# Optimization experiments

Measured on AMD Instinct MI355X. Metric: run time of the kernel, lower is better.

## Reference

```python
import jax, jax.numpy as jnp
import numpy as np

U = 512   # units
D = 512   # decoder input feature dim
V = 46    # output vocab


def _lstm_cell(x_t, h, c, W, R, b):
    # Keras LSTMCell: gate order i, f, g(cell), o; sigmoid recurrent act, tanh act.
    z = x_t @ W + h @ R + b                      # [B, 4U]
    i, f, g, o = jnp.split(z, 4, axis=-1)
    i = jax.nn.sigmoid(i)
    f = jax.nn.sigmoid(f)
    g = jnp.tanh(g)
    o = jax.nn.sigmoid(o)
    c_new = f * c + i * g
    h_new = o * jnp.tanh(c_new)
    return h_new, c_new


def _lstm_seq(seq, W, R, b):
    # seq: [T, B, D]; zero initial state (Keras default). Returns (all h [T,B,U], last h [B,U]).
    B = seq.shape[1]
    u = R.shape[0]
    h0 = jnp.zeros((B, u), seq.dtype)
    c0 = jnp.zeros((B, u), seq.dtype)
    def step(carry, x_t):
        h, c = carry
        h, c = _lstm_cell(x_t, h, c, W, R, b)
        return (h, c), h
    (hT, _), hs = jax.lax.scan(step, (h0, c0), seq)
    return hs, hT


def setup_inputs() -> dict:
    key = jax.random.key(0)
    ks = jax.random.split(key, 10)
    def p(k, shape, scale=0.05):
        return jax.random.normal(k, shape, dtype=jnp.float32) * scale
    x = jax.random.normal(ks[0], (32, 512, U), dtype=jnp.float32)   # encoder outputs [B, S, U]
    y = jax.random.normal(ks[1], (32, 128, D), dtype=jnp.float32)   # decoder inputs  [B, T, D]
    return {
        "x": x, "y": y,
        "W_a": p(ks[2], (D, 4 * U)), "R_a": p(ks[3], (U, 4 * U)), "b_a": jnp.zeros((4 * U,), jnp.float32),
        "W1": p(ks[4], (U, 4 * U)), "R1": p(ks[5], (U, 4 * U)), "b1": jnp.zeros((4 * U,), jnp.float32),
        "W2": p(ks[6], (U, 4 * U)), "R2": p(ks[7], (U, 4 * U)), "b2": jnp.zeros((4 * U,), jnp.float32),
        "Wd": p(ks[8], (U, V)), "bd": jnp.zeros((V,), jnp.float32),
    }


def reference(x, y, W_a, R_a, b_a, W1, R1, b1, W2, R2, b2, Wd, bd):
    B = y.shape[0]
    yT = jnp.swapaxes(y, 0, 1)                          # [T, B, D]
    h0 = jnp.zeros((B, U), x.dtype)
    c0 = jnp.zeros((B, U), x.dtype)

    # AttentionLSTM: per-step LSTMCell + dot-product attention (Keras Attention,
    # unscaled, keys==values==x) + residual add of the context into both states.
    def step(carry, y_t):
        h, c = carry
        h, c = _lstm_cell(y_t, h, c, W_a, R_a, b_a)     # s = h  [B, U]
        scores = jnp.einsum('bu,bsu->bs', h, x)         # [B, S]
        ctx = jnp.einsum('bs,bsu->bu', jax.nn.softmax(scores, axis=-1), x)  # [B, U]
        return (h + ctx, c + ctx), ctx

    _, ctxs = jax.lax.scan(step, (h0, c0), yT)          # [T, B, U]

    # Stacked LSTMs: first returns full sequence, second returns last hidden state.
    hs1, _ = _lstm_seq(ctxs, W1, R1, b1)                # [T, B, U]
    _, hT = _lstm_seq(hs1, W2, R2, b2)                  # [B, U]

    logits = hT @ Wd + bd                               # [B, V]
    return jax.nn.softmax(logits, axis=-1)
```

## Files before the change

### kernel.cpp

```cpp
#include <hip/hip_runtime.h>
#include <math.h>


#define U_   512
#define S_   512
#define T_   128
#define B_   32
#define G4   2048
#define V_   46
#define NWG  256
#define FSTR 32

#define AT_LD(p)     __hip_atomic_load((p), __ATOMIC_RELAXED, __HIP_MEMORY_SCOPE_AGENT)
#define AT_ST(p, v)  __hip_atomic_store((p), (v), __ATOMIC_RELAXED, __HIP_MEMORY_SCOPE_AGENT)

__device__ __forceinline__ void group_bar(unsigned* gflags, unsigned seq) {
  __syncthreads();
  const int tid = threadIdx.x;
  if (tid < 32) {
    if (tid == 0)
      AT_ST(&gflags[(blockIdx.x & 31) * FSTR], seq);
    while (!__all(AT_LD(&gflags[tid * FSTR]) >= seq))
      __builtin_amdgcn_s_sleep(1);
  }
  __syncthreads();
}

__global__ __launch_bounds__(256) void gemm_k512(
    const float* __restrict__ A, const float* __restrict__ W,
    const float* __restrict__ b, float* __restrict__ Z) {
  const int tid = threadIdx.x;
  const int j = blockIdx.x * 1024 + tid * 4;
  const int i0 = blockIdx.y * 8;
  float4 bj = *(const float4*)(b + j);
  float4 acc[8];
#pragma unroll
  for (int r = 0; r < 8; ++r) acc[r] = bj;
  const float* Arow = A + (size_t)i0 * U_;
  for (int k = 0; k < U_; ++k) {
    float4 w = *(const float4*)(W + (size_t)k * G4 + j);
#pragma unroll
    for (int r = 0; r < 8; ++r) {
      float a = Arow[(size_t)r * U_ + k];
      acc[r].x = fmaf(a, w.x, acc[r].x);
      acc[r].y = fmaf(a, w.y, acc[r].y);
      acc[r].z = fmaf(a, w.z, acc[r].z);
      acc[r].w = fmaf(a, w.w, acc[r].w);
    }
  }
#pragma unroll
  for (int r = 0; r < 8; ++r)
    *(float4*)(Z + (size_t)(i0 + r) * G4 + j) = acc[r];
}

__global__ __launch_bounds__(256) void transpose_R(
    const float* __restrict__ R, float* __restrict__ RT) {
  __shared__ float tile[64][65];
  const int c0 = blockIdx.x * 64, k0 = blockIdx.y * 64;
  const int tc = threadIdx.x & 63, tr = threadIdx.x >> 6;
  for (int r = tr; r < 64; r += 4)
    tile[r][tc] = R[(size_t)(k0 + r) * G4 + c0 + tc];
  __syncthreads();
  for (int r = tr; r < 64; r += 4)
    RT[(size_t)(c0 + r) * 512 + k0 + tc] = tile[tc][r];
}

__global__ __launch_bounds__(512) void attn_coop(
    const float* __restrict__ x, const float* __restrict__ ZY,
    const float* __restrict__ RT, float* __restrict__ ctxs,
    float* hbuf, float* hnbuf, float* smax, float* ssumg,
    float* ctxpart, unsigned* flags) {
  extern __shared__ float dyn[];
  float* x_s  = dyn;
  float* h_st = dyn + 512 * 65;
  __shared__ float zp[4][64][2];
  __shared__ float hn_s[512];
  __shared__ float p_s[64];
  __shared__ float ctx_s[64];

  const int tid = threadIdx.x;
  const int bid = blockIdx.x;
  const int g    = bid >> 5;
  const int wgid = bid & 31;
  const int u0   = wgid * 16;
  const int kh  = tid & 1;
  const int b_l = (tid >> 1) & 3;
  const int col = tid >> 3;
  const int zcol = (col >> 4) * 512 + u0 + (col & 15);
  const int b_att = 4 * g + (wgid >> 3);
  const int sc = wgid & 7;
  unsigned* gflags = flags + g * 32 * FSTR;

  for (int idx = tid; idx < 64 * 512; idx += 512) {
    int sl = idx >> 9, u = idx & 511;
    x_s[u * 65 + sl] = x[((size_t)b_att * S_ + sc * 64 + sl) * U_ + u];
  }
  float c = 0.f, hn_reg = 0.f;
  unsigned seq = 0;
  __syncthreads();

  for (int t = 0; t < T_; ++t) {
    {
      const float4* hb4 =
          (const float4*)(hbuf + (size_t)t * 16384 + 4 * g * 512);
      float4 v = hb4[tid];
      *(float4*)(h_st + (tid >> 7) * 516 + (tid & 127) * 4) = v;
    }
    __syncthreads();
    {
      const float4* H4 = (const float4*)(h_st + b_l * 516 + kh * 256);
      const float4* R4 = (const float4*)(RT + (size_t)zcol * 512 + kh * 256);
      float acc = 0.f;
#pragma unroll 8
      for (int i = 0; i < 64; ++i) {
        float4 hv = H4[i];
        float4 rv = R4[i];
        acc = fmaf(hv.x, rv.x, acc); acc = fmaf(hv.y, rv.y, acc);
        acc = fmaf(hv.z, rv.z, acc); acc = fmaf(hv.w, rv.w, acc);
      }
      zp[b_l][col][kh] = acc;
    }
    __syncthreads();
    if (tid < 64) {
      const int bb = tid >> 4, uu = tid & 15;
      const int b = 4 * g + bb, u = u0 + uu;
      const float* zy = ZY + ((size_t)b * T_ + t) * G4 + u;
      float zi = zy[0]    + zp[bb][uu][0]      + zp[bb][uu][1];
      float zf = zy[512]  + zp[bb][16 + uu][0] + zp[bb][16 + uu][1];
      float zg = zy[1024] + zp[bb][32 + uu][0] + zp[bb][32 + uu][1];
      float zo = zy[1536] + zp[bb][48 + uu][0] + zp[bb][48 + uu][1];
      float ig = 1.f / (1.f + expf(-zi));
      float fg = 1.f / (1.f + expf(-zf));
      float gg = tanhf(zg);
      float og = 1.f / (1.f + expf(-zo));
      c = fg * c + ig * gg;
      hn_reg = og * tanhf(c);
      AT_ST(&hnbuf[(size_t)t * 16384 + b * 512 + u], hn_reg);
    }
    group_bar(gflags, ++seq);

    if (tid < 128) {
      float4 v = ((const float4*)(hnbuf + (size_t)t * 16384 + b_att * 512))[tid];
      *(float4*)(hn_s + tid * 4) = v;
    }
    __syncthreads();
    {
      const int wv = tid >> 6, ln = tid & 63;
      for (int si = 0; si < 8; ++si) {
        const int sl = wv * 8 + si;
        float a = 0.f;
#pragma unroll
        for (int uu = ln; uu < 512; uu += 64)
          a = fmaf(hn_s[uu], x_s[uu * 65 + sl], a);
#pragma unroll
        for (int off = 32; off; off >>= 1) a += __shfl_down(a, off);
        if (ln == 0) p_s[sl] = a;
      }
    }
    __syncthreads();
    if (tid < 64) {
      float v = p_s[tid];
      float m = v;
#pragma unroll
      for (int off = 32; off; off >>= 1) m = fmaxf(m, __shfl_down(m, off));
      m = __shfl(m, 0);
      float ex = expf(v - m);
      p_s[tid] = ex;
      float sm = ex;
#pragma unroll
      for (int off = 32; off; off >>= 1) sm += __shfl_down(sm, off);
      if (tid == 0) {
        AT_ST(&smax[b_att * 8 + sc], m);
        AT_ST(&ssumg[b_att * 8 + sc], sm);
      }
    }
    __syncthreads();
    {
      float a = 0.f;
      const float* xr = x_s + tid * 65;
#pragma unroll 8
      for (int s = 0; s < 64; ++s) a = fmaf(p_s[s], xr[s], a);
      AT_ST(&ctxpart[((size_t)b_att * 8 + sc) * 512 + tid], a);
    }
    group_bar(gflags, ++seq);

    {
      const int j = tid & 7;
      const int pair = tid >> 3;
      const int bb = pair >> 4, uu = pair & 15;
      const int b = 4 * g + bb, u = u0 + uu;
      float lm = AT_LD(&smax[b * 8 + j]);
      float ss = AT_LD(&ssumg[b * 8 + j]);
      float cp = AT_LD(&ctxpart[((size_t)b * 8 + j) * 512 + u]);
      float gm = lm;
#pragma unroll
      for (int off = 1; off < 8; off <<= 1)
        gm = fmaxf(gm, __shfl_xor(gm, off));
      float w = expf(lm - gm);
      float st = ss * w, cs = cp * w;
#pragma unroll
      for (int off = 1; off < 8; off <<= 1) {
        st += __shfl_xor(st, off);
        cs += __shfl_xor(cs, off);
      }
      if (j == 0) ctx_s[pair] = cs / st;
    }
    __syncthreads();
    if (tid < 64) {
      const int bb = tid >> 4, uu = tid & 15;
      const int b = 4 * g + bb, u = u0 + uu;
      float ctxv = ctx_s[tid];
      c += ctxv;
      float hcar = hn_reg + ctxv;
      AT_ST(&hbuf[(size_t)(t + 1) * 16384 + b * 512 + u], hcar);
      ctxs[((size_t)b * T_ + t) * U_ + u] = ctxv;
    }
    group_bar(gflags, ++seq);
  }
}

__global__ __launch_bounds__(512) void lstm_coop(
    const float* __restrict__ Zin, const float* __restrict__ R,
    float* __restrict__ seq_out, float* __restrict__ last_out,
    float* hbuf, unsigned* flags) {
  extern __shared__ float dyn[];
  float* R_s  = dyn;
  float* h_st = dyn + 64 * 516;
  __shared__ float zp[4][64][2];
  const int tid = threadIdx.x;
  const int bid = blockIdx.x;
  const int g    = bid >> 5;
  const int wgid = bid & 31;
  const int u0   = wgid * 16;
  const int kh  = tid & 1;
  const int b_l = (tid >> 1) & 3;
  const int col = tid >> 3;
  unsigned* gflags = flags + g * 32 * FSTR;

  for (int idx = tid; idx < 64 * 512; idx += 512) {
    int cc = idx & 63, kk = idx >> 6;
    R_s[cc * 516 + kk] = R[(size_t)kk * G4 + (cc >> 4) * 512 + u0 + (cc & 15)];
  }
  float c = 0.f;
  unsigned seq = 0;
  __syncthreads();

  for (int t = 0; t < T_; ++t) {
    {
      const float4* hb4 =
          (const float4*)(hbuf + (size_t)t * 16384 + 4 * g * 512);
      float4 v = hb4[tid];
      *(float4*)(h_st + (tid >> 7) * 516 + (tid & 127) * 4) = v;
    }
    __syncthreads();
    {
      const float4* H4 = (const float4*)(h_st + b_l * 516 + kh * 256);
      const float4* R4 = (const float4*)(R_s + col * 516 + kh * 256);
      float acc = 0.f;
#pragma unroll 8
      for (int i = 0; i < 64; ++i) {
        float4 hv = H4[i];
        float4 rv = R4[i];
        acc = fmaf(hv.x, rv.x, acc); acc = fmaf(hv.y, rv.y, acc);
        acc = fmaf(hv.z, rv.z, acc); acc = fmaf(hv.w, rv.w, acc);
      }
      zp[b_l][col][kh] = acc;
    }
    __syncthreads();
    if (tid < 64) {
      const int bb = tid >> 4, uu = tid & 15;
      const int b = 4 * g + bb, u = u0 + uu;
      const float* zy = Zin + ((size_t)b * T_ + t) * G4 + u;
      float zi = zy[0]    + zp[bb][uu][0]      + zp[bb][uu][1];
      float zf = zy[512]  + zp[bb][16 + uu][0] + zp[bb][16 + uu][1];
      float zg = zy[1024] + zp[bb][32 + uu][0] + zp[bb][32 + uu][1];
      float zo = zy[1536] + zp[bb][48 + uu][0] + zp[bb][48 + uu][1];
      float ig = 1.f / (1.f + expf(-zi));
      float fg = 1.f / (1.f + expf(-zf));
      float gg = tanhf(zg);
      float og = 1.f / (1.f + expf(-zo));
      c = fg * c + ig * gg;
      float hv2 = og * tanhf(c);
      AT_ST(&hbuf[(size_t)(t + 1) * 16384 + b * 512 + u], hv2);
      if (seq_out) seq_out[((size_t)b * T_ + t) * U_ + u] = hv2;
      if (last_out && t == T_ - 1) last_out[b * U_ + u] = hv2;
    }
    group_bar(gflags, ++seq);
  }
}

__global__ __launch_bounds__(64) void final_k(
    const float* __restrict__ hT, const float* __restrict__ Wd,
    const float* __restrict__ bd, float* __restrict__ out) {
  const int b = blockIdx.x;
  const int v = threadIdx.x;
  float acc = (v < V_) ? bd[v] : -INFINITY;
  if (v < V_) {
    for (int k = 0; k < U_; ++k)
      acc = fmaf(hT[(size_t)b * U_ + k], Wd[(size_t)k * V_ + v], acc);
  }
  float m = acc;
#pragma unroll
  for (int off = 32; off; off >>= 1) m = fmaxf(m, __shfl_down(m, off));
  m = __shfl(m, 0);
  float e = (v < V_) ? expf(acc - m) : 0.f;
  float s = e;
#pragma unroll
  for (int off = 32; off; off >>= 1) s += __shfl_down(s, off);
  s = __shfl(s, 0);
  if (v < V_) out[(size_t)b * V_ + v] = e / s;
}

extern "C" void kernel_launch(void* const* d_in, const int* in_sizes, int n_in,
                              void* d_out, int out_size, void* d_ws, size_t ws_size,
                              hipStream_t stream) {
  const float* x   = (const float*)d_in[0];
  const float* y   = (const float*)d_in[1];
  const float* W_a = (const float*)d_in[2];
  const float* R_a = (const float*)d_in[3];
  const float* b_a = (const float*)d_in[4];
  const float* W1  = (const float*)d_in[5];
  const float* R1  = (const float*)d_in[6];
  const float* b1  = (const float*)d_in[7];
  const float* W2  = (const float*)d_in[8];
  const float* R2  = (const float*)d_in[9];
  const float* b2  = (const float*)d_in[10];
  const float* Wd  = (const float*)d_in[11];
  const float* bd  = (const float*)d_in[12];
  float* out = (float*)d_out;

  float* ZBUF  = (float*)d_ws;
  float* SEQ   = ZBUF + (size_t)8388608;
  float* RT    = SEQ + (size_t)2097152;
  float* HROT  = RT + (size_t)1048576;
  float* HNROT = HROT + (size_t)2113536;
  float* SMAX  = HNROT + (size_t)2097152;
  float* SSUM  = SMAX + 256;
  float* CTXP  = SSUM + 256;
  float* HT    = CTXP + 131072;
  unsigned* BAR = (unsigned*)(HT + 16384);

  const int REGION = 8 * 32 * FSTR;
  unsigned* FLG_A = BAR;
  unsigned* FLG_1 = BAR + REGION;
  unsigned* FLG_2 = BAR + 2 * REGION;

  const int attn_lds = (512 * 65 + 4 * 516) * 4;
  const int lstm_lds = (64 * 516 + 4 * 516) * 4;
  hipFuncSetAttribute((const void*)attn_coop,
                      hipFuncAttributeMaxDynamicSharedMemorySize, attn_lds);
  hipFuncSetAttribute((const void*)lstm_coop,
                      hipFuncAttributeMaxDynamicSharedMemorySize, lstm_lds);

  dim3 ggrid(2, 512);
  hipMemsetAsync(BAR, 0, 3 * REGION * 4, stream);

  gemm_k512<<<ggrid, 256, 0, stream>>>(y, W_a, b_a, ZBUF);
  transpose_R<<<dim3(32, 8), 256, 0, stream>>>(R_a, RT);
  hipMemsetAsync(HROT, 0, 16384 * 4, stream);
  attn_coop<<<NWG, 512, attn_lds, stream>>>(x, ZBUF, RT, SEQ, HROT, HNROT,
                                            SMAX, SSUM, CTXP, FLG_A);
  gemm_k512<<<ggrid, 256, 0, stream>>>(SEQ, W1, b1, ZBUF);
  hipMemsetAsync(HROT, 0, 16384 * 4, stream);
  lstm_coop<<<NWG, 512, lstm_lds, stream>>>(ZBUF, R1, SEQ, nullptr, HROT,
                                            FLG_1);
  gemm_k512<<<ggrid, 256, 0, stream>>>(SEQ, W2, b2, ZBUF);
  hipMemsetAsync(HROT, 0, 16384 * 4, stream);
  lstm_coop<<<NWG, 512, lstm_lds, stream>>>(ZBUF, R2, nullptr, HT, HROT,
                                            FLG_2);
  final_k<<<B_, 64, 0, stream>>>(HT, Wd, bd, out);
}
```

Measured before the change: 4.047 ms.

## Drop per-step grid barrier by redundantly reducing context in every workgroup

```diff
diff --git a/kernel.cpp b/kernel.cpp
--- a/kernel.cpp
+++ b/kernel.cpp
@@ -68,15 +68,16 @@
 __global__ __launch_bounds__(512) void attn_coop(
     const float* __restrict__ x, const float* __restrict__ ZY,
     const float* __restrict__ RT, float* __restrict__ ctxs,
-    float* hbuf, float* hnbuf, float* smax, float* ssumg,
+    float* hnbuf, float* smax, float* ssumg,
     float* ctxpart, unsigned* flags) {
   extern __shared__ float dyn[];
   float* x_s  = dyn;
   float* h_st = dyn + 512 * 65;
   __shared__ float zp[4][64][2];
-  __shared__ float hn_s[512];
   __shared__ float p_s[64];
   __shared__ float ctx_s[64];
+  __shared__ float w_s[4][8];
+  __shared__ float st_s[4];
 
   const int tid = threadIdx.x;
   const int bid = blockIdx.x;
@@ -95,18 +96,12 @@
     int sl = idx >> 9, u = idx & 511;
     x_s[u * 65 + sl] = x[((size_t)b_att * S_ + sc * 64 + sl) * U_ + u];
   }
-  float c = 0.f, hn_reg = 0.f;
+  for (int i = tid; i < 4 * 516; i += 512) h_st[i] = 0.f;
+  float c = 0.f;
   unsigned seq = 0;
   __syncthreads();
 
   for (int t = 0; t < T_; ++t) {
-    {
-      const float4* hb4 =
-          (const float4*)(hbuf + (size_t)t * 16384 + 4 * g * 512);
-      float4 v = hb4[tid];
-      *(float4*)(h_st + (tid >> 7) * 516 + (tid & 127) * 4) = v;
-    }
-    __syncthreads();
     {
       const float4* H4 = (const float4*)(h_st + b_l * 516 + kh * 256);
       const float4* R4 = (const float4*)(RT + (size_t)zcol * 512 + kh * 256);
@@ -134,24 +129,23 @@
       float gg = tanhf(zg);
       float og = 1.f / (1.f + expf(-zo));
       c = fg * c + ig * gg;
-      hn_reg = og * tanhf(c);
+      float hn_reg = og * tanhf(c);
       AT_ST(&hnbuf[(size_t)t * 16384 + b * 512 + u], hn_reg);
     }
     group_bar(gflags, ++seq);
 
-    if (tid < 128) {
-      float4 v = ((const float4*)(hnbuf + (size_t)t * 16384 + b_att * 512))[tid];
-      *(float4*)(hn_s + tid * 4) = v;
-    }
-    __syncthreads();
     {
       const int wv = tid >> 6, ln = tid & 63;
+      const float* hnb = hnbuf + (size_t)t * 16384 + b_att * 512;
+      float hreg[8];
+#pragma unroll
+      for (int k = 0; k < 8; ++k) hreg[k] = hnb[ln + 64 * k];
       for (int si = 0; si < 8; ++si) {
         const int sl = wv * 8 + si;
         float a = 0.f;
 #pragma unroll
-        for (int uu = ln; uu < 512; uu += 64)
-          a = fmaf(hn_s[uu], x_s[uu * 65 + sl], a);
+        for (int k = 0; k < 8; ++k)
+          a = fmaf(hreg[k], x_s[(ln + 64 * k) * 65 + sl], a);
 #pragma unroll
         for (int off = 32; off; off >>= 1) a += __shfl_down(a, off);
         if (ln == 0) p_s[sl] = a;
@@ -185,25 +179,49 @@
     group_bar(gflags, ++seq);
 
     {
-      const int j = tid & 7;
-      const int pair = tid >> 3;
-      const int bb = pair >> 4, uu = pair & 15;
-      const int b = 4 * g + bb, u = u0 + uu;
-      float lm = AT_LD(&smax[b * 8 + j]);
-      float ss = AT_LD(&ssumg[b * 8 + j]);
-      float cp = AT_LD(&ctxpart[((size_t)b * 8 + j) * 512 + u]);
-      float gm = lm;
-#pragma unroll
-      for (int off = 1; off < 8; off <<= 1)
-        gm = fmaxf(gm, __shfl_xor(gm, off));
-      float w = expf(lm - gm);
-      float st = ss * w, cs = cp * w;
-#pragma unroll
-      for (int off = 1; off < 8; off <<= 1) {
-        st += __shfl_xor(st, off);
-        cs += __shfl_xor(cs, off);
-      }
-      if (j == 0) ctx_s[pair] = cs / st;
+      const int bb = tid >> 7;
+      const int u4 = (tid & 127) * 4;
+      const int b = 4 * g + bb;
+      float lm = 0.f, ss = 0.f;
+      if (tid < 32) {
+        lm = AT_LD(&smax[(4 * g + (tid >> 3)) * 8 + (tid & 7)]);
+        ss = AT_LD(&ssumg[(4 * g + (tid >> 3)) * 8 + (tid & 7)]);
+      }
+      float4 hn4 = *(const float4*)(hnbuf + (size_t)t * 16384 + b * 512 + u4);
+      float cpv[8][4];
+#pragma unroll
+      for (int j = 0; j < 8; ++j) {
+        const float* cp = ctxpart + ((size_t)b * 8 + j) * 512 + u4;
+#pragma unroll
+        for (int k = 0; k < 4; ++k) cpv[j][k] = AT_LD(cp + k);
+      }
+      if (tid < 32) {
+        float gm = lm;
+#pragma unroll
+        for (int off = 1; off < 8; off <<= 1)
+          gm = fmaxf(gm, __shfl_xor(gm, off));
+        float w = expf(lm - gm);
+        float st = ss * w;
+#pragma unroll
+        for (int off = 1; off < 8; off <<= 1) st += __shfl_xor(st, off);
+        w_s[tid >> 3][tid & 7] = w;
+        if ((tid & 7) == 0) st_s[tid >> 3] = st;
+      }
+      __syncthreads();
+      float cx0 = 0.f, cx1 = 0.f, cx2 = 0.f, cx3 = 0.f;
+#pragma unroll
+      for (int j = 0; j < 8; ++j) {
+        float wj = w_s[bb][j];
+        cx0 = fmaf(wj, cpv[j][0], cx0);
+        cx1 = fmaf(wj, cpv[j][1], cx1);
+        cx2 = fmaf(wj, cpv[j][2], cx2);
+        cx3 = fmaf(wj, cpv[j][3], cx3);
+      }
+      float st = st_s[bb];
+      float4 cxv = {cx0 / st, cx1 / st, cx2 / st, cx3 / st};
+      float4 hv = {hn4.x + cxv.x, hn4.y + cxv.y, hn4.z + cxv.z, hn4.w + cxv.w};
+      *(float4*)(h_st + bb * 516 + u4) = hv;
+      if ((u4 >> 4) == wgid) *(float4*)(ctx_s + bb * 16 + (u4 & 15)) = cxv;
     }
     __syncthreads();
     if (tid < 64) {
@@ -211,11 +229,8 @@
       const int b = 4 * g + bb, u = u0 + uu;
       float ctxv = ctx_s[tid];
       c += ctxv;
-      float hcar = hn_reg + ctxv;
-      AT_ST(&hbuf[(size_t)(t + 1) * 16384 + b * 512 + u], hcar);
       ctxs[((size_t)b * T_ + t) * U_ + u] = ctxv;
     }
-    group_bar(gflags, ++seq);
   }
 }
 
@@ -357,8 +372,7 @@
 
   gemm_k512<<<ggrid, 256, 0, stream>>>(y, W_a, b_a, ZBUF);
   transpose_R<<<dim3(32, 8), 256, 0, stream>>>(R_a, RT);
-  hipMemsetAsync(HROT, 0, 16384 * 4, stream);
-  attn_coop<<<NWG, 512, attn_lds, stream>>>(x, ZBUF, RT, SEQ, HROT, HNROT,
+  attn_coop<<<NWG, 512, attn_lds, stream>>>(x, ZBUF, RT, SEQ, HNROT,
                                             SMAX, SSUM, CTXP, FLG_A);
   gemm_k512<<<ggrid, 256, 0, stream>>>(SEQ, W1, b1, ZBUF);
   hipMemsetAsync(HROT, 0, 16384 * 4, stream);
```

Measured after the change: 4.279 ms. 5.7% more time.

## Double workgroup count for attention and LSTM recurrent kernels

Applied to the files above, without the earlier changes.

```diff
diff --git a/kernel.cpp b/kernel.cpp
--- a/kernel.cpp
+++ b/kernel.cpp
@@ -8,18 +8,19 @@
 #define B_   32
 #define G4   2048
 #define V_   46
-#define NWG  256
 #define FSTR 32
 
 #define AT_LD(p)     __hip_atomic_load((p), __ATOMIC_RELAXED, __HIP_MEMORY_SCOPE_AGENT)
 #define AT_ST(p, v)  __hip_atomic_store((p), (v), __ATOMIC_RELAXED, __HIP_MEMORY_SCOPE_AGENT)
 
-__device__ __forceinline__ void group_bar(unsigned* gflags, unsigned seq) {
+template <int NW>
+__device__ __forceinline__ void group_bar(unsigned* gflags, unsigned seq,
+                                          int wgid) {
   __syncthreads();
   const int tid = threadIdx.x;
-  if (tid < 32) {
+  if (tid < NW) {
     if (tid == 0)
-      AT_ST(&gflags[(blockIdx.x & 31) * FSTR], seq);
+      AT_ST(&gflags[wgid * FSTR], seq);
     while (!__all(AT_LD(&gflags[tid * FSTR]) >= seq))
       __builtin_amdgcn_s_sleep(1);
   }
@@ -72,47 +73,48 @@
     float* ctxpart, unsigned* flags) {
   extern __shared__ float dyn[];
   float* x_s  = dyn;
-  float* h_st = dyn + 512 * 65;
-  __shared__ float zp[4][64][2];
-  __shared__ float hn_s[512];
-  __shared__ float p_s[64];
-  __shared__ float ctx_s[64];
+  float* h_st = dyn + 512 * 33;
+  __shared__ float zp[2][64][4];
+  __shared__ float p_s[32];
+  __shared__ float ctx_s[32];
 
   const int tid = threadIdx.x;
   const int bid = blockIdx.x;
   const int g    = bid >> 5;
   const int wgid = bid & 31;
   const int u0   = wgid * 16;
-  const int kh  = tid & 1;
-  const int b_l = (tid >> 1) & 3;
+  const int kh  = tid & 3;
+  const int b_l = (tid >> 2) & 1;
   const int col = tid >> 3;
   const int zcol = (col >> 4) * 512 + u0 + (col & 15);
-  const int b_att = 4 * g + (wgid >> 3);
-  const int sc = wgid & 7;
+  const int b_att = 2 * g + (wgid >> 4);
+  const int sc = wgid & 15;
   unsigned* gflags = flags + g * 32 * FSTR;
 
-  for (int idx = tid; idx < 64 * 512; idx += 512) {
+  for (int idx = tid; idx < 32 * 512; idx += 512) {
     int sl = idx >> 9, u = idx & 511;
-    x_s[u * 65 + sl] = x[((size_t)b_att * S_ + sc * 64 + sl) * U_ + u];
+    x_s[u * 33 + sl] = x[((size_t)b_att * S_ + sc * 32 + sl) * U_ + u];
   }
   float c = 0.f, hn_reg = 0.f;
   unsigned seq = 0;
   __syncthreads();
 
   for (int t = 0; t < T_; ++t) {
-    {
+    if (tid < 256) {
       const float4* hb4 =
-          (const float4*)(hbuf + (size_t)t * 16384 + 4 * g * 512);
+          (const float4*)(hbuf + (size_t)t * 16384 + 2 * g * 512);
       float4 v = hb4[tid];
-      *(float4*)(h_st + (tid >> 7) * 516 + (tid & 127) * 4) = v;
-    }
-    __syncthreads();
-    {
-      const float4* H4 = (const float4*)(h_st + b_l * 516 + kh * 256);
-      const float4* R4 = (const float4*)(RT + (size_t)zcol * 512 + kh * 256);
+      int b = tid >> 7;
+      int kk4 = (tid & 127) * 4;
+      *(float4*)(h_st + b * 516 + (kk4 >> 7) * 129 + (kk4 & 127)) = v;
+    }
+    __syncthreads();
+    {
+      const float4* H4 = (const float4*)(h_st + b_l * 516 + kh * 129);
+      const float4* R4 = (const float4*)(RT + (size_t)zcol * 512 + kh * 128);
       float acc = 0.f;
 #pragma unroll 8
-      for (int i = 0; i < 64; ++i) {
+      for (int i = 0; i < 32; ++i) {
         float4 hv = H4[i];
         float4 rv = R4[i];
         acc = fmaf(hv.x, rv.x, acc); acc = fmaf(hv.y, rv.y, acc);
@@ -121,14 +123,18 @@
       zp[b_l][col][kh] = acc;
     }
     __syncthreads();
-    if (tid < 64) {
+    if (tid < 32) {
       const int bb = tid >> 4, uu = tid & 15;
-      const int b = 4 * g + bb, u = u0 + uu;
+      const int b = 2 * g + bb, u = u0 + uu;
       const float* zy = ZY + ((size_t)b * T_ + t) * G4 + u;
-      float zi = zy[0]    + zp[bb][uu][0]      + zp[bb][uu][1];
-      float zf = zy[512]  + zp[bb][16 + uu][0] + zp[bb][16 + uu][1];
-      float zg = zy[1024] + zp[bb][32 + uu][0] + zp[bb][32 + uu][1];
-      float zo = zy[1536] + zp[bb][48 + uu][0] + zp[bb][48 + uu][1];
+      float zi = zy[0]    + zp[bb][uu][0]      + zp[bb][uu][1]
+                          + zp[bb][uu][2]      + zp[bb][uu][3];
+      float zf = zy[512]  + zp[bb][16 + uu][0] + zp[bb][16 + uu][1]
+                          + zp[bb][16 + uu][2] + zp[bb][16 + uu][3];
+      float zg = zy[1024] + zp[bb][32 + uu][0] + zp[bb][32 + uu][1]
+                          + zp[bb][32 + uu][2] + zp[bb][32 + uu][3];
+      float zo = zy[1536] + zp[bb][48 + uu][0] + zp[bb][48 + uu][1]
+                          + zp[bb][48 + uu][2] + zp[bb][48 + uu][3];
       float ig = 1.f / (1.f + expf(-zi));
       float fg = 1.f / (1.f + expf(-zf));
       float gg = tanhf(zg);
@@ -137,85 +143,84 @@
       hn_reg = og * tanhf(c);
       AT_ST(&hnbuf[(size_t)t * 16384 + b * 512 + u], hn_reg);
     }
-    group_bar(gflags, ++seq);
-
-    if (tid < 128) {
-      float4 v = ((const float4*)(hnbuf + (size_t)t * 16384 + b_att * 512))[tid];
-      *(float4*)(hn_s + tid * 4) = v;
-    }
-    __syncthreads();
+    group_bar<32>(gflags, ++seq, wgid);
+
     {
       const int wv = tid >> 6, ln = tid & 63;
-      for (int si = 0; si < 8; ++si) {
-        const int sl = wv * 8 + si;
+      const float* hnb = hnbuf + (size_t)t * 16384 + b_att * 512;
+      float hreg[8];
+#pragma unroll
+      for (int k = 0; k < 8; ++k) hreg[k] = hnb[ln + 64 * k];
+      for (int si = 0; si < 4; ++si) {
+        const int sl = wv * 4 + si;
         float a = 0.f;
 #pragma unroll
-        for (int uu = ln; uu < 512; uu += 64)
-          a = fmaf(hn_s[uu], x_s[uu * 65 + sl], a);
+        for (int k = 0; k < 8; ++k)
+          a = fmaf(hreg[k], x_s[(ln + 64 * k) * 33 + sl], a);
 #pragma unroll
         for (int off = 32; off; off >>= 1) a += __shfl_down(a, off);
         if (ln == 0) p_s[sl] = a;
       }
     }
     __syncthreads();
-    if (tid < 64) {
+    if (tid < 32) {
       float v = p_s[tid];
       float m = v;
 #pragma unroll
-      for (int off = 32; off; off >>= 1) m = fmaxf(m, __shfl_down(m, off));
+      for (int off = 16; off; off >>= 1) m = fmaxf(m, __shfl_down(m, off));
       m = __shfl(m, 0);
       float ex = expf(v - m);
       p_s[tid] = ex;
       float sm = ex;
 #pragma unroll
-      for (int off = 32; off; off >>= 1) sm += __shfl_down(sm, off);
+      for (int off = 16; off; off >>= 1) sm += __shfl_down(sm, off);
       if (tid == 0) {
-        AT_ST(&smax[b_att * 8 + sc], m);
-        AT_ST(&ssumg[b_att * 8 + sc], sm);
+        AT_ST(&smax[b_att * 16 + sc], m);
+        AT_ST(&ssumg[b_att * 16 + sc], sm);
       }
     }
     __syncthreads();
     {
       float a = 0.f;
-      const float* xr = x_s + tid * 65;
+      const float* xr = x_s + tid * 33;
 #pragma unroll 8
-      for (int s = 0; s < 64; ++s) a = fmaf(p_s[s], xr[s], a);
-      AT_ST(&ctxpart[((size_t)b_att * 8 + sc) * 512 + tid], a);
-    }
-    group_bar(gflags, ++seq);
-
-    {
-      const int j = tid & 7;
-      const int pair = tid >> 3;
+      for (int s = 0; s < 32; ++s) a = fmaf(p_s[s], xr[s], a);
+      AT_ST(&ctxpart[((size_t)b_att * 16 + sc) * 512 + tid], a);
+    }
+    group_bar<32>(gflags, ++seq, wgid);
+
+    {
+      const int j = tid & 15;
+      const int pair = tid >> 4;
       const int bb = pair >> 4, uu = pair & 15;
-      const int b = 4 * g + bb, u = u0 + uu;
-      float lm = AT_LD(&smax[b * 8 + j]);
-      float ss = AT_LD(&ssumg[b * 8 + j]);
-      float cp = AT_LD(&ctxpart[((size_t)b * 8 + j) * 512 + u]);
+      const int b = 2 * g + bb, u = u0 + uu;
+      float lm = AT_LD(&smax[b * 16 + j]);
+      float ss = AT_LD(&ssumg[b * 16 + j]);
+      float cp = AT_LD(&ctxpart[((size_t)b * 16 + j) * 512 + u]);
       float gm = lm;
 #pragma unroll
-      for (int off = 1; off < 8; off <<= 1)
+      for (int off = 1; off < 16; off <<= 1)
         gm = fmaxf(gm, __shfl_xor(gm, off));
       float w = expf(lm - gm);
       float st = ss * w, cs = cp * w;
 #pragma unroll
-      for (int off = 1; off < 8; off <<= 1) {
+      for (int off = 1; off < 16; off <<= 1) {
         st += __shfl_xor(st, off);
         cs += __shfl_xor(cs, off);
       }
       if (j == 0) ctx_s[pair] = cs / st;
     }
     __syncthreads();
-    if (tid < 64) {
+    if (tid < 32) {
       const int bb = tid >> 4, uu = tid & 15;
-      const int b = 4 * g + bb, u = u0 + uu;
+      const int b = 2 * g + bb, u = u0 + uu;
       float ctxv = ctx_s[tid];
       c += ctxv;
       float hcar = hn_reg + ctxv;
       AT_ST(&hbuf[(size_t)(t + 1) * 16384 + b * 512 + u], hcar);
       ctxs[((size_t)b * T_ + t) * U_ + u] = ctxv;
     }
-    group_bar(gflags, ++seq);
+    group_bar<32>(gflags, ++seq, wgid);
   }
 }
 
@@ -225,21 +230,22 @@
     float* hbuf, unsigned* flags) {
   extern __shared__ float dyn[];
   float* R_s  = dyn;
-  float* h_st = dyn + 64 * 516;
-  __shared__ float zp[4][64][2];
+  float* h_st = dyn + 32 * 516;
+  __shared__ float zp[4][32][4];
   const int tid = threadIdx.x;
   const int bid = blockIdx.x;
-  const int g    = bid >> 5;
-  const int wgid = bid & 31;
-  const int u0   = wgid * 16;
-  const int kh  = tid & 1;
-  const int b_l = (tid >> 1) & 3;
-  const int col = tid >> 3;
-  unsigned* gflags = flags + g * 32 * FSTR;
-
-  for (int idx = tid; idx < 64 * 512; idx += 512) {
-    int cc = idx & 63, kk = idx >> 6;
-    R_s[cc * 516 + kk] = R[(size_t)kk * G4 + (cc >> 4) * 512 + u0 + (cc & 15)];
+  const int g    = bid >> 6;
+  const int wgid = bid & 63;
+  const int u0   = wgid * 8;
+  const int kh  = tid & 3;
+  const int b_l = (tid >> 2) & 3;
+  const int col = tid >> 4;
+  unsigned* gflags = flags + g * 64 * FSTR;
+
+  for (int idx = tid; idx < 32 * 512; idx += 512) {
+    int cc = idx & 31, kk = idx >> 5;
+    R_s[cc * 516 + (kk >> 7) * 129 + (kk & 127)] =
+        R[(size_t)kk * G4 + (cc >> 3) * 512 + u0 + (cc & 7)];
   }
   float c = 0.f;
   unsigned seq = 0;
@@ -250,15 +256,17 @@
       const float4* hb4 =
           (const float4*)(hbuf + (size_t)t * 16384 + 4 * g * 512);
       float4 v = hb4[tid];
-      *(float4*)(h_st + (tid >> 7) * 516 + (tid & 127) * 4) = v;
-    }
-    __syncthreads();
-    {
-      const float4* H4 = (const float4*)(h_st + b_l * 516 + kh * 256);
-      const float4* R4 = (const float4*)(R_s + col * 516 + kh * 256);
+      int b = tid >> 7;
+      int kk4 = (tid & 127) * 4;
+      *(float4*)(h_st + b * 516 + (kk4 >> 7) * 129 + (kk4 & 127)) = v;
+    }
+    __syncthreads();
+    {
+      const float4* H4 = (const float4*)(h_st + b_l * 516 + kh * 129);
+      const float4* R4 = (const float4*)(R_s + col * 516 + kh * 129);
       float acc = 0.f;
 #pragma unroll 8
-      for (int i = 0; i < 64; ++i) {
+      for (int i = 0; i < 32; ++i) {
         float4 hv = H4[i];
         float4 rv = R4[i];
         acc = fmaf(hv.x, rv.x, acc); acc = fmaf(hv.y, rv.y, acc);
@@ -267,14 +275,18 @@
       zp[b_l][col][kh] = acc;
     }
     __syncthreads();
-    if (tid < 64) {
-      const int bb = tid >> 4, uu = tid & 15;
+    if (tid < 32) {
+      const int bb = tid >> 3, uu = tid & 7;
       const int b = 4 * g + bb, u = u0 + uu;
       const float* zy = Zin + ((size_t)b * T_ + t) * G4 + u;
-      float zi = zy[0]    + zp[bb][uu][0]      + zp[bb][uu][1];
-      float zf = zy[512]  + zp[bb][16 + uu][0] + zp[bb][16 + uu][1];
-      float zg = zy[1024] + zp[bb][32 + uu][0] + zp[bb][32 + uu][1];
-      float zo = zy[1536] + zp[bb][48 + uu][0] + zp[bb][48 + uu][1];
+      float zi = zy[0]    + zp[bb][uu][0]      + zp[bb][uu][1]
+                          + zp[bb][uu][2]      + zp[bb][uu][3];
+      float zf = zy[512]  + zp[bb][8 + uu][0]  + zp[bb][8 + uu][1]
+                          + zp[bb][8 + uu][2]  + zp[bb][8 + uu][3];
+      float zg = zy[1024] + zp[bb][16 + uu][0] + zp[bb][16 + uu][1]
+                          + zp[bb][16 + uu][2] + zp[bb][16 + uu][3];
+      float zo = zy[1536] + zp[bb][24 + uu][0] + zp[bb][24 + uu][1]
+                          + zp[bb][24 + uu][2] + zp[bb][24 + uu][3];
       float ig = 1.f / (1.f + expf(-zi));
       float fg = 1.f / (1.f + expf(-zf));
       float gg = tanhf(zg);
@@ -285,7 +297,7 @@
       if (seq_out) seq_out[((size_t)b * T_ + t) * U_ + u] = hv2;
       if (last_out && t == T_ - 1) last_out[b * U_ + u] = hv2;
     }
-    group_bar(gflags, ++seq);
+    group_bar<64>(gflags, ++seq, wgid);
   }
 }
 
@@ -335,18 +347,18 @@
   float* HROT  = RT + (size_t)1048576;
   float* HNROT = HROT + (size_t)2113536;
   float* SMAX  = HNROT + (size_t)2097152;
-  float* SSUM  = SMAX + 256;
-  float* CTXP  = SSUM + 256;
-  float* HT    = CTXP + 131072;
+  float* SSUM  = SMAX + 1024;
+  float* CTXP  = SSUM + 1024;
+  float* HT    = CTXP + 262144;
   unsigned* BAR = (unsigned*)(HT + 16384);
 
-  const int REGION = 8 * 32 * FSTR;
+  const int REGION = 16384;
   unsigned* FLG_A = BAR;
   unsigned* FLG_1 = BAR + REGION;
   unsigned* FLG_2 = BAR + 2 * REGION;
 
-  const int attn_lds = (512 * 65 + 4 * 516) * 4;
-  const int lstm_lds = (64 * 516 + 4 * 516) * 4;
+  const int attn_lds = (512 * 33 + 2 * 516) * 4;
+  const int lstm_lds = (32 * 516 + 4 * 516) * 4;
   hipFuncSetAttribute((const void*)attn_coop,
                       hipFuncAttributeMaxDynamicSharedMemorySize, attn_lds);
   hipFuncSetAttribute((const void*)lstm_coop,
@@ -358,15 +370,15 @@
   gemm_k512<<<ggrid, 256, 0, stream>>>(y, W_a, b_a, ZBUF);
   transpose_R<<<dim3(32, 8), 256, 0, stream>>>(R_a, RT);
   hipMemsetAsync(HROT, 0, 16384 * 4, stream);
-  attn_coop<<<NWG, 512, attn_lds, stream>>>(x, ZBUF, RT, SEQ, HROT, HNROT,
+  attn_coop<<<512, 512, attn_lds, stream>>>(x, ZBUF, RT, SEQ, HROT, HNROT,
                                             SMAX, SSUM, CTXP, FLG_A);
   gemm_k512<<<ggrid, 256, 0, stream>>>(SEQ, W1, b1, ZBUF);
   hipMemsetAsync(HROT, 0, 16384 * 4, stream);
-  lstm_coop<<<NWG, 512, lstm_lds, stream>>>(ZBUF, R1, SEQ, nullptr, HROT,
+  lstm_coop<<<512, 512, lstm_lds, stream>>>(ZBUF, R1, SEQ, nullptr, HROT,
                                             FLG_1);
   gemm_k512<<<ggrid, 256, 0, stream>>>(SEQ, W2, b2, ZBUF);
   hipMemsetAsync(HROT, 0, 16384 * 4, stream);
-  lstm_coop<<<NWG, 512, lstm_lds, stream>>>(ZBUF, R2, nullptr, HT, HROT,
+  lstm_coop<<<512, 512, lstm_lds, stream>>>(ZBUF, R2, nullptr, HT, HROT,
                                             FLG_2);
   final_k<<<B_, 64, 0, stream>>>(HT, Wd, bd, out);
 }
```

After: 11.05 ms. 2.73x slower.

## Fuse both stacked LSTM layers into one wavefront-pipelined persistent kernel

Applied to the files above, without the earlier changes.

```diff
diff --git a/kernel.cpp b/kernel.cpp
--- a/kernel.cpp
+++ b/kernel.cpp
@@ -14,16 +14,31 @@
 #define AT_LD(p)     __hip_atomic_load((p), __ATOMIC_RELAXED, __HIP_MEMORY_SCOPE_AGENT)
 #define AT_ST(p, v)  __hip_atomic_store((p), (v), __ATOMIC_RELAXED, __HIP_MEMORY_SCOPE_AGENT)
 
-__device__ __forceinline__ void group_bar(unsigned* gflags, unsigned seq) {
+__device__ __forceinline__ void group_bar(unsigned* gflags, unsigned seq,
+                                          int wgid) {
   __syncthreads();
   const int tid = threadIdx.x;
   if (tid < 32) {
     if (tid == 0)
-      AT_ST(&gflags[(blockIdx.x & 31) * FSTR], seq);
+      AT_ST(&gflags[wgid * FSTR], seq);
     while (!__all(AT_LD(&gflags[tid * FSTR]) >= seq))
       __builtin_amdgcn_s_sleep(1);
   }
   __syncthreads();
+}
+
+__device__ __forceinline__ void g_wait32(unsigned* gflags, unsigned seq) {
+  if (threadIdx.x < 32) {
+    while (!__all(AT_LD(&gflags[threadIdx.x * FSTR]) >= seq))
+      __builtin_amdgcn_s_sleep(1);
+  }
+  __syncthreads();
+}
+
+__device__ __forceinline__ void g_arrive(unsigned* gflags, unsigned seq,
+                                         int wgid) {
+  __syncthreads();
+  if (threadIdx.x == 0) AT_ST(&gflags[wgid * FSTR], seq);
 }
 
 __global__ __launch_bounds__(256) void gemm_k512(
@@ -137,7 +152,7 @@
       hn_reg = og * tanhf(c);
       AT_ST(&hnbuf[(size_t)t * 16384 + b * 512 + u], hn_reg);
     }
-    group_bar(gflags, ++seq);
+    group_bar(gflags, ++seq, wgid);
 
     if (tid < 128) {
       float4 v = ((const float4*)(hnbuf + (size_t)t * 16384 + b_att * 512))[tid];
@@ -182,7 +197,7 @@
       for (int s = 0; s < 64; ++s) a = fmaf(p_s[s], xr[s], a);
       AT_ST(&ctxpart[((size_t)b_att * 8 + sc) * 512 + tid], a);
     }
-    group_bar(gflags, ++seq);
+    group_bar(gflags, ++seq, wgid);
 
     {
       const int j = tid & 7;
@@ -215,77 +230,145 @@
       AT_ST(&hbuf[(size_t)(t + 1) * 16384 + b * 512 + u], hcar);
       ctxs[((size_t)b * T_ + t) * U_ + u] = ctxv;
     }
-    group_bar(gflags, ++seq);
-  }
-}
-
-__global__ __launch_bounds__(512) void lstm_coop(
-    const float* __restrict__ Zin, const float* __restrict__ R,
-    float* __restrict__ seq_out, float* __restrict__ last_out,
-    float* hbuf, unsigned* flags) {
+    group_bar(gflags, ++seq, wgid);
+  }
+}
+
+__global__ __launch_bounds__(512) void lstm_fused(
+    const float* __restrict__ Z1, const float* __restrict__ R1,
+    const float* __restrict__ R2, const float* __restrict__ W2T,
+    const float* __restrict__ b2, float* h1rot, float* h2rot,
+    float* __restrict__ hT, unsigned* fl1, unsigned* fl2) {
   extern __shared__ float dyn[];
   float* R_s  = dyn;
   float* h_st = dyn + 64 * 516;
-  __shared__ float zp[4][64][2];
+  __shared__ float zp[8][64];
+
   const int tid = threadIdx.x;
   const int bid = blockIdx.x;
-  const int g    = bid >> 5;
-  const int wgid = bid & 31;
-  const int u0   = wgid * 16;
-  const int kh  = tid & 1;
-  const int b_l = (tid >> 1) & 3;
-  const int col = tid >> 3;
-  unsigned* gflags = flags + g * 32 * FSTR;
-
+  const int layer = bid >> 7;
+  const int g     = (bid >> 5) & 3;
+  const int wgid  = bid & 31;
+  const int u0    = wgid * 16;
+  const int b_l   = tid & 7;
+  const int col   = tid >> 3;
+  const int zcol  = (col >> 4) * 512 + u0 + (col & 15);
+  unsigned* own = (layer ? fl2 : fl1) + g * 32 * FSTR;
+  unsigned* in1 = fl1 + g * 32 * FSTR;
+
+  const float* Rm = layer ? R2 : R1;
   for (int idx = tid; idx < 64 * 512; idx += 512) {
     int cc = idx & 63, kk = idx >> 6;
-    R_s[cc * 516 + kk] = R[(size_t)kk * G4 + (cc >> 4) * 512 + u0 + (cc & 15)];
+    R_s[cc * 516 + kk] = Rm[(size_t)kk * G4 + (cc >> 4) * 512 + u0 + (cc & 15)];
   }
   float c = 0.f;
-  unsigned seq = 0;
-  __syncthreads();
-
-  for (int t = 0; t < T_; ++t) {
-    {
-      const float4* hb4 =
-          (const float4*)(hbuf + (size_t)t * 16384 + 4 * g * 512);
-      float4 v = hb4[tid];
-      *(float4*)(h_st + (tid >> 7) * 516 + (tid & 127) * 4) = v;
-    }
-    __syncthreads();
-    {
-      const float4* H4 = (const float4*)(h_st + b_l * 516 + kh * 256);
-      const float4* R4 = (const float4*)(R_s + col * 516 + kh * 256);
-      float acc = 0.f;
+  __syncthreads();
+
+  if (layer == 0) {
+    for (int t = 0; t < T_; ++t) {
+      {
+        const float4* hb4 =
+            (const float4*)(h1rot + (size_t)t * 16384 + (size_t)(8 * g) * 512);
+#pragma unroll
+        for (int it = 0; it < 2; ++it) {
+          int idx = it * 512 + tid;
+          float4 v = hb4[idx];
+          *(float4*)(h_st + (idx >> 7) * 516 + (idx & 127) * 4) = v;
+        }
+      }
+      __syncthreads();
+      {
+        const float4* H4 = (const float4*)(h_st + b_l * 516);
+        const float4* Rr = (const float4*)(R_s + col * 516);
+        float acc = 0.f;
 #pragma unroll 8
-      for (int i = 0; i < 64; ++i) {
-        float4 hv = H4[i];
-        float4 rv = R4[i];
-        acc = fmaf(hv.x, rv.x, acc); acc = fmaf(hv.y, rv.y, acc);
-        acc = fmaf(hv.z, rv.z, acc); acc = fmaf(hv.w, rv.w, acc);
-      }
-      zp[b_l][col][kh] = acc;
-    }
-    __syncthreads();
-    if (tid < 64) {
-      const int bb = tid >> 4, uu = tid & 15;
-      const int b = 4 * g + bb, u = u0 + uu;
-      const float* zy = Zin + ((size_t)b * T_ + t) * G4 + u;
-      float zi = zy[0]    + zp[bb][uu][0]      + zp[bb][uu][1];
-      float zf = zy[512]  + zp[bb][16 + uu][0] + zp[bb][16 + uu][1];
-      float zg = zy[1024] + zp[bb][32 + uu][0] + zp[bb][32 + uu][1];
-      float zo = zy[1536] + zp[bb][48 + uu][0] + zp[bb][48 + uu][1];
-      float ig = 1.f / (1.f + expf(-zi));
-      float fg = 1.f / (1.f + expf(-zf));
-      float gg = tanhf(zg);
-      float og = 1.f / (1.f + expf(-zo));
-      c = fg * c + ig * gg;
-      float hv2 = og * tanhf(c);
-      AT_ST(&hbuf[(size_t)(t + 1) * 16384 + b * 512 + u], hv2);
-      if (seq_out) seq_out[((size_t)b * T_ + t) * U_ + u] = hv2;
-      if (last_out && t == T_ - 1) last_out[b * U_ + u] = hv2;
-    }
-    group_bar(gflags, ++seq);
+        for (int i = 0; i < 128; ++i) {
+          float4 hv = H4[i];
+          float4 rv = Rr[i];
+          acc = fmaf(hv.x, rv.x, acc); acc = fmaf(hv.y, rv.y, acc);
+          acc = fmaf(hv.z, rv.z, acc); acc = fmaf(hv.w, rv.w, acc);
+        }
+        zp[b_l][col] = acc;
+      }
+      __syncthreads();
+      if (tid < 128) {
+        const int bb = tid >> 4, uu = tid & 15;
+        const int b = 8 * g + bb, u = u0 + uu;
+        const float* zy = Z1 + ((size_t)b * T_ + t) * G4 + u;
+        float zi = zy[0]    + zp[bb][uu];
+        float zf = zy[512]  + zp[bb][16 + uu];
+        float zg = zy[1024] + zp[bb][32 + uu];
+        float zo = zy[1536] + zp[bb][48 + uu];
+        float ig = 1.f / (1.f + expf(-zi));
+        float fg = 1.f / (1.f + expf(-zf));
+        float gg = tanhf(zg);
+        float og = 1.f / (1.f + expf(-zo));
+        c = fg * c + ig * gg;
+        float hv2 = og * tanhf(c);
+        AT_ST(&h1rot[(size_t)(t + 1) * 16384 + (size_t)b * 512 + u], hv2);
+      }
+      group_bar(own, t + 1, wgid);
+    }
+  } else {
+    for (int t = 0; t < T_; ++t) {
+      g_wait32(in1, t + 1);
+      float accW = 0.f;
+      {
+        const float4* W4 = (const float4*)(W2T + (size_t)zcol * 512);
+        const float4* H1 = (const float4*)(h1rot + (size_t)(t + 1) * 16384 +
+                                           (size_t)(8 * g + b_l) * 512);
+#pragma unroll 4
+        for (int i = 0; i < 128; ++i) {
+          float4 wv = W4[i];
+          float4 hv = H1[i];
+          accW = fmaf(hv.x, wv.x, accW); accW = fmaf(hv.y, wv.y, accW);
+          accW = fmaf(hv.z, wv.z, accW); accW = fmaf(hv.w, wv.w, accW);
+        }
+      }
+      if (t) g_wait32(own, t);
+      {
+        const float4* hb4 =
+            (const float4*)(h2rot + (size_t)t * 16384 + (size_t)(8 * g) * 512);
+#pragma unroll
+        for (int it = 0; it < 2; ++it) {
+          int idx = it * 512 + tid;
+          float4 v = hb4[idx];
+          *(float4*)(h_st + (idx >> 7) * 516 + (idx & 127) * 4) = v;
+        }
+      }
+      __syncthreads();
+      {
+        const float4* H4 = (const float4*)(h_st + b_l * 516);
+        const float4* Rr = (const float4*)(R_s + col * 516);
+        float acc = accW;
+#pragma unroll 8
+        for (int i = 0; i < 128; ++i) {
+          float4 hv = H4[i];
+          float4 rv = Rr[i];
+          acc = fmaf(hv.x, rv.x, acc); acc = fmaf(hv.y, rv.y, acc);
+          acc = fmaf(hv.z, rv.z, acc); acc = fmaf(hv.w, rv.w, acc);
+        }
+        zp[b_l][col] = acc;
+      }
+      __syncthreads();
+      if (tid < 128) {
+        const int bb = tid >> 4, uu = tid & 15;
+        const int b = 8 * g + bb, u = u0 + uu;
+        float zi = b2[u]        + zp[bb][uu];
+        float zf = b2[512 + u]  + zp[bb][16 + uu];
+        float zg = b2[1024 + u] + zp[bb][32 + uu];
+        float zo = b2[1536 + u] + zp[bb][48 + uu];
+        float ig = 1.f / (1.f + expf(-zi));
+        float fg = 1.f / (1.f + expf(-zf));
+        float gg = tanhf(zg);
+        float og = 1.f / (1.f + expf(-zo));
+        c = fg * c + ig * gg;
+        float hv2 = og * tanhf(c);
+        AT_ST(&h2rot[(size_t)(t + 1) * 16384 + (size_t)b * 512 + u], hv2);
+        if (t == T_ - 1) hT[(size_t)b * 512 + u] = hv2;
+      }
+      g_arrive(own, t + 1, wgid);
+    }
   }
 }
 
@@ -338,19 +421,22 @@
   float* SSUM  = SMAX + 256;
   float* CTXP  = SSUM + 256;
   float* HT    = CTXP + 131072;
-  unsigned* BAR = (unsigned*)(HT + 16384);
+  float* H2ROT = HT + 16384;
+  unsigned* BAR = (unsigned*)(H2ROT + 2113536);
+
+  float* W2T = HNROT;
 
   const int REGION = 8 * 32 * FSTR;
   unsigned* FLG_A = BAR;
   unsigned* FLG_1 = BAR + REGION;
   unsigned* FLG_2 = BAR + 2 * REGION;
 
-  const int attn_lds = (512 * 65 + 4 * 516) * 4;
-  const int lstm_lds = (64 * 516 + 4 * 516) * 4;
+  const int attn_lds  = (512 * 65 + 4 * 516) * 4;
+  const int fused_lds = (64 * 516 + 8 * 516) * 4;
   hipFuncSetAttribute((const void*)attn_coop,
                       hipFuncAttributeMaxDynamicSharedMemorySize, attn_lds);
-  hipFuncSetAttribute((const void*)lstm_coop,
-                      hipFuncAttributeMaxDynamicSharedMemorySize, lstm_lds);
+  hipFuncSetAttribute((const void*)lstm_fused,
+                      hipFuncAttributeMaxDynamicSharedMemorySize, fused_lds);
 
   dim3 ggrid(2, 512);
   hipMemsetAsync(BAR, 0, 3 * REGION * 4, stream);
@@ -361,12 +447,10 @@
   attn_coop<<<NWG, 512, attn_lds, stream>>>(x, ZBUF, RT, SEQ, HROT, HNROT,
                                             SMAX, SSUM, CTXP, FLG_A);
   gemm_k512<<<ggrid, 256, 0, stream>>>(SEQ, W1, b1, ZBUF);
+  transpose_R<<<dim3(32, 8), 256, 0, stream>>>(W2, W2T);
   hipMemsetAsync(HROT, 0, 16384 * 4, stream);
-  lstm_coop<<<NWG, 512, lstm_lds, stream>>>(ZBUF, R1, SEQ, nullptr, HROT,
-                                            FLG_1);
-  gemm_k512<<<ggrid, 256, 0, stream>>>(SEQ, W2, b2, ZBUF);
-  hipMemsetAsync(HROT, 0, 16384 * 4, stream);
-  lstm_coop<<<NWG, 512, lstm_lds, stream>>>(ZBUF, R2, nullptr, HT, HROT,
-                                            FLG_2);
+  hipMemsetAsync(H2ROT, 0, 16384 * 4, stream);
+  lstm_fused<<<NWG, 512, fused_lds, stream>>>(ZBUF, R1, R2, W2T, b2,
+                                              HROT, H2ROT, HT, FLG_1, FLG_2);
   final_k<<<B_, 64, 0, stream>>>(HT, Wd, bd, out);
 }
```

After: 7.675 ms. 1.9x slower.
